# Optimization experiments

Hardware: AMD Instinct MI355X
Metric: run time of the kernel (lower is better)

Reference implementation:

```python
import jax, jax.numpy as jnp
import numpy as np
from jax import lax

# Conv4d decomposed (as in the torch implementation) into a sum of Conv3d's
# over the first spatial kernel axis. Each 3D conv is vectorized by folding
# the strided first-dim slices into the batch dimension.

def conv4d(x, w, b, stride=(2, 2, 2, 2), padding=(1, 1, 1, 1)):
    # x: [B, Ci, D1, D2, D3, D4]; w: [Co, Ci, K1, K2, K3, K4]; b: [Co]
    B, Ci, D1, D2, D3, D4 = x.shape
    Co, _, K1, K2, K3, K4 = w.shape
    s1, p1 = stride[0], padding[0]
    T = (D1 + 2 * p1 - K1) // s1 + 1  # output size along first spatial dim
    xp = jnp.pad(x, ((0, 0), (0, 0), (p1, p1), (0, 0), (0, 0), (0, 0)))
    pad3 = [(padding[j], padding[j]) for j in (1, 2, 3)]
    out = None
    for i in range(K1):  # small fixed loop over kernel taps along dim0
        xi = xp[:, :, i:i + s1 * (T - 1) + 1:s1]           # [B, Ci, T, D2, D3, D4]
        xi = jnp.moveaxis(xi, 2, 1).reshape(B * T, Ci, D2, D3, D4)
        yi = lax.conv_general_dilated(
            xi, w[:, :, i], window_strides=stride[1:], padding=pad3,
            dimension_numbers=('NCDHW', 'OIDHW', 'NCDHW'))
        out = yi if out is None else out + yi
    O2, O3, O4 = out.shape[2], out.shape[3], out.shape[4]
    out = out.reshape(B, T, Co, O2, O3, O4)
    out = jnp.moveaxis(out, 1, 2)                          # [B, Co, T, O2, O3, O4]
    return out + b[None, :, None, None, None, None]


def setup_inputs() -> dict:
    key = jax.random.key(0)
    k0, k1, k2, k3, k4 = jax.random.split(key, 5)
    C, R = 16, 4  # in_channel, mlp_ratio
    H = C * R     # 64
    x = jax.random.normal(k0, (1, C, 32, 32, 32, 32), dtype=jnp.float32)
    w1 = jax.random.normal(k1, (H, C, 3, 3, 3, 3), dtype=jnp.float32) * 0.02
    b1 = jax.random.normal(k2, (H,), dtype=jnp.float32) * 0.02
    w2 = jax.random.normal(k3, (C, H, 3, 3, 3, 3), dtype=jnp.float32) * 0.02
    b2 = jax.random.normal(k4, (C,), dtype=jnp.float32) * 0.02
    return {'x': x, 'w1': w1, 'b1': b1, 'w2': w2, 'b2': b2}


def reference(x, w1, b1, w2, b2):
    h = conv4d(x, w1, b1)                      # [1, 64, 16, 16, 16, 16]
    h = jax.nn.gelu(h, approximate=False)      # exact erf GELU (torch default)
    return conv4d(h, w2, b2)                   # [1, 16, 8, 8, 8, 8]
```

## Files before the change

### kernel.cpp

```cpp
#include <hip/hip_runtime.h>
#include <hip/hip_bf16.h>
#include <math.h>


typedef __attribute__((ext_vector_type(8))) short short8;
typedef __attribute__((ext_vector_type(4))) float f32x4;
typedef __attribute__((ext_vector_type(4))) unsigned int uint4v;

__device__ __forceinline__ unsigned short f2bf(float v) {
    __hip_bfloat16 b = __float2bfloat16(v);
    return *(unsigned short*)&b;
}

__global__ void setup_kernel(const float* __restrict__ w1, const float* __restrict__ w2,
                             const float* __restrict__ b2,
                             unsigned short* __restrict__ w1p, unsigned short* __restrict__ w2p,
                             uint4v* __restrict__ hz, float* __restrict__ out) {
    int b = blockIdx.x, tid = threadIdx.x;
    if (b < 544) {
        int i = b * 256 + tid;
        int kp = i % 136, co = (i / 136) & 63, ci = i / 8704;
        float v = 0.f;
        if (kp < 108 && (kp & 3) < 3) v = w1[(co * 16 + ci) * 81 + (kp >> 2) * 3 + (kp & 3)];
        w1p[i] = f2bf(v);
    } else if (b < 1088) {
        int i = (b - 544) * 256 + tid;
        int kp = i % 136, co = (i / 136) & 15, ci = i / 2176;
        float v = 0.f;
        if (kp < 108 && (kp & 3) < 3) v = w2[(co * 64 + ci) * 81 + (kp >> 2) * 3 + (kp & 3)];
        w2p[i] = f2bf(v);
    } else if (b < 1344) {
        int i = (b - 1088) * 256 + tid;
        out[i] = b2[i >> 12];
    } else {
        int i = (b - 1344) * 256 + tid;
        hz[i] = (uint4v){0, 0, 0, 0};
        int j = i + 704512;
        if (j < 839808) hz[j] = (uint4v){0, 0, 0, 0};
    }
}

__global__ __launch_bounds__(256) void conv1_mfma(
        const float* __restrict__ x, const unsigned short* __restrict__ w1p,
        const float* __restrict__ b1, unsigned short* __restrict__ hpad) {
    __shared__ unsigned short sX[36000];

    const int tid = threadIdx.x;
    const int bid = blockIdx.x;
    const int t4 = bid & 1, t3 = (bid >> 1) & 7, t2 = (bid >> 4) & 7, t1 = bid >> 7;
    const int bo1 = 2 * t1, bo2 = 2 * t2, bo3 = 2 * t3, bo4 = 8 * t4;
    const int g1b = 2 * bo1 - 1, g2b = 2 * bo2 - 1, g3b = 2 * bo3 - 1, g4b = 2 * bo4 - 1;

    int offs[5], swb[5];
    unsigned mka = 0, mkb = 0;
#pragma unroll
    for (int r = 0; r < 5; ++r) {
        int u = tid + 256 * r;
        bool uok = u < 1125;
        int uu = uok ? u : 0;
        int p = uu % 9, q = uu / 9;
        int i3 = q % 5; q /= 5;
        int i2 = q % 5; int i1 = q / 5;
        int g1 = g1b + i1, g2 = g2b + i2, g3 = g3b + i3;
        bool ok123 = uok & ((unsigned)g1 < 32u) & ((unsigned)g2 < 32u) & ((unsigned)g3 < 32u);
        int g4a = g4b + 2 * p;
        offs[r] = ((g1 * 32 + g2) * 32 + g3) * 32 + g4a;
        if (ok123 && (unsigned)g4a < 32u) mka |= 1u << r;
        if (ok123 && (unsigned)(g4a + 1) < 32u) mkb |= 1u << r;
        swb[r] = 2 * (((i1 * 5 + i2) * 5 + i3) * 18 + 2 * p);
    }

    {
        float fa[5], fb[5], na[5], nb[5];
#pragma unroll
        for (int r = 0; r < 5; ++r) {
            float va = 0.f, vb = 0.f;
            if ((mka >> r) & 1) va = x[offs[r]];
            if ((mkb >> r) & 1) vb = x[offs[r] + 1];
            fa[r] = va; fb[r] = vb;
        }
        for (int ci = 0; ci < 16; ++ci) {
            if (ci < 15) {
                const float* xc = x + (size_t)(ci + 1) * 1048576;
#pragma unroll
                for (int r = 0; r < 5; ++r) {
                    float va = 0.f, vb = 0.f;
                    if ((mka >> r) & 1) va = xc[offs[r]];
                    if ((mkb >> r) & 1) vb = xc[offs[r] + 1];
                    na[r] = va; nb[r] = vb;
                }
            }
            char* slab = (char*)sX + ci * 4500;
#pragma unroll
            for (int r = 0; r < 4; ++r)
                *(unsigned*)(slab + swb[r]) =
                    (unsigned)f2bf(fa[r]) | ((unsigned)f2bf(fb[r]) << 16);
            if (tid < 101)
                *(unsigned*)(slab + swb[4]) =
                    (unsigned)f2bf(fa[4]) | ((unsigned)f2bf(fb[4]) << 16);
            if (ci < 15) {
#pragma unroll
                for (int r = 0; r < 5; ++r) { fa[r] = na[r]; fb[r] = nb[r]; }
            }
        }
    }
    __syncthreads();

    const int lane = tid & 63, wv = tid >> 6;
    const int n16 = lane & 15, hi = lane >> 4;
    const int ct0 = 2 * (wv & 1);
    const int st0 = 2 * (wv >> 1);

    int fpb[2];
#pragma unroll
    for (int tt = 0; tt < 2; ++tt) {
        int sp = (st0 + tt) * 16 + n16;
        int o4l = sp & 7, o3l = (sp >> 3) & 1, o2l = (sp >> 4) & 1, o1l = sp >> 5;
        fpb[tt] = 2 * (900 * o1l + 180 * o2l + 36 * o3l + 2 * o4l);
    }
    int kof[4][2];
#pragma unroll
    for (int ks = 0; ks < 4; ++ks)
#pragma unroll
    for (int j = 0; j < 2; ++j) {
        int g = 8 * ks + 2 * hi + j;
        if (g > 26) g = 26;
        int k1 = g / 9, k2 = (g / 3) % 3, k3 = g % 3;
        kof[ks][j] = 2 * (450 * k1 + 90 * k2 + 18 * k3);
    }

    auto loadA = [&](int ci, short8 (&Ac)[8]) {
        const unsigned short* aw0 = w1p + (size_t)(ci * 64 + 16 * ct0 + n16) * 136 + hi * 8;
#pragma unroll
        for (int k = 0; k < 4; ++k) Ac[k] = *(const short8*)(aw0 + 32 * k);
        const unsigned short* aw1 = aw0 + 16 * 136;
#pragma unroll
        for (int k = 0; k < 4; ++k) Ac[4 + k] = *(const short8*)(aw1 + 32 * k);
    };

    f32x4 acc[2][2];
#pragma unroll
    for (int c = 0; c < 2; ++c)
#pragma unroll
    for (int t = 0; t < 2; ++t) acc[c][t] = (f32x4){0.f, 0.f, 0.f, 0.f};

    short8 A0[8], A1[8];
    loadA(0, A0);
    loadA(1, A1);

    auto kbody = [&](int ci, short8 (&Ac)[8]) {
        const char* sx = (const char*)sX + ci * 4500;
        short8 fr[2][4];
#pragma unroll
        for (int tt = 0; tt < 2; ++tt) {
            const char* base = sx + fpb[tt];
#pragma unroll
            for (int ks = 0; ks < 4; ++ks) {
                unsigned r0 = *(const unsigned*)(base + kof[ks][0]);
                unsigned r1 = *(const unsigned*)(base + kof[ks][0] + 4);
                unsigned r2 = *(const unsigned*)(base + kof[ks][1]);
                unsigned r3 = *(const unsigned*)(base + kof[ks][1] + 4);
                uint4v tmp = (uint4v){r0, r1, r2, r3};
                fr[tt][ks] = *(short8*)&tmp;
            }
        }
#pragma unroll
        for (int tt = 0; tt < 2; ++tt)
#pragma unroll
        for (int ks = 0; ks < 4; ++ks) {
            acc[0][tt] = __builtin_amdgcn_mfma_f32_16x16x32_bf16(Ac[ks],     fr[tt][ks], acc[0][tt], 0, 0, 0);
            acc[1][tt] = __builtin_amdgcn_mfma_f32_16x16x32_bf16(Ac[4 + ks], fr[tt][ks], acc[1][tt], 0, 0, 0);
        }
        if (ci < 14) loadA(ci + 2, Ac);
    };

    for (int cc = 0; cc < 16; cc += 2) {
        kbody(cc, A0);
        kbody(cc + 1, A1);
    }

#pragma unroll
    for (int c = 0; c < 2; ++c) {
#pragma unroll
        for (int tt = 0; tt < 2; ++tt) {
            int spl = 16 * (st0 + tt) + n16;
            int e4 = spl & 7, e3 = (spl >> 3) & 1, e2 = (spl >> 4) & 1, e1 = spl >> 5;
            size_t base = (size_t)(bo1 + e1 + 1) * 5832 + (bo2 + e2 + 1) * 324 +
                          (bo3 + e3 + 1) * 18 + (bo4 + e4 + 1);
#pragma unroll
            for (int r = 0; r < 4; ++r) {
                int co = 16 * (ct0 + c) + 4 * hi + r;
                float v = acc[c][tt][r] + b1[co];
                v = 0.5f * v * (1.f + erff(v * 0.70710678118654752f));
                hpad[(size_t)co * 104976 + base] = f2bf(v);
            }
        }
    }
}

__global__ __launch_bounds__(256) void conv2_mfma(
        const unsigned short* __restrict__ hpad, const unsigned short* __restrict__ w2p,
        float* __restrict__ out) {
    __shared__ unsigned short sX[18000];

    const int tid = threadIdx.x;
    const int bid = blockIdx.x;
    const int s = bid & 63, cig = bid >> 6;
    const int t3 = s & 3, t2 = (s >> 2) & 3, t1 = s >> 4;
    const int bo1 = 2 * t1, bo2 = 2 * t2, bo3 = 2 * t3;

    int offs[5], swb[5];
#pragma unroll
    for (int r = 0; r < 5; ++r) {
        int u = tid + 256 * r;
        if (u >= 1125) u = 0;
        int p = u % 9, q = u / 9;
        int i3 = q % 5; q /= 5;
        int i2 = q % 5; int i1 = q / 5;
        offs[r] = (2 * bo1 + i1) * 5832 + (2 * bo2 + i2) * 324 + (2 * bo3 + i3) * 18 + 2 * p;
        swb[r] = 2 * (((i1 * 5 + i2) * 5 + i3) * 18 + 2 * p);
    }

    {
        unsigned fa[5], na[5];
        const unsigned short* h0 = hpad + (size_t)(cig * 8) * 104976;
#pragma unroll
        for (int r = 0; r < 5; ++r) fa[r] = *(const unsigned*)(h0 + offs[r]);
        for (int s8 = 0; s8 < 8; ++s8) {
            if (s8 < 7) {
                const unsigned short* hc = hpad + (size_t)(cig * 8 + s8 + 1) * 104976;
#pragma unroll
                for (int r = 0; r < 5; ++r) na[r] = *(const unsigned*)(hc + offs[r]);
            }
            char* slab = (char*)sX + s8 * 4500;
#pragma unroll
            for (int r = 0; r < 4; ++r) *(unsigned*)(slab + swb[r]) = fa[r];
            if (tid < 101) *(unsigned*)(slab + swb[4]) = fa[4];
            if (s8 < 7) {
#pragma unroll
                for (int r = 0; r < 5; ++r) fa[r] = na[r];
            }
        }
    }
    __syncthreads();

    const int lane = tid & 63, wv = tid >> 6;
    const int n16 = lane & 15, hi = lane >> 4;

    int fpb;
    {
        int sp = wv * 16 + n16;
        int o4l = sp & 7, o3l = (sp >> 3) & 1, o2l = (sp >> 4) & 1, o1l = sp >> 5;
        fpb = 2 * (900 * o1l + 180 * o2l + 36 * o3l + 2 * o4l);
    }
    int kof[4][2];
#pragma unroll
    for (int ks = 0; ks < 4; ++ks)
#pragma unroll
    for (int j = 0; j < 2; ++j) {
        int g = 8 * ks + 2 * hi + j;
        if (g > 26) g = 26;
        int k1 = g / 9, k2 = (g / 3) % 3, k3 = g % 3;
        kof[ks][j] = 2 * (450 * k1 + 90 * k2 + 18 * k3);
    }

    auto loadA = [&](int s8, short8 (&Ac)[4]) {
        const unsigned short* aw = w2p + (size_t)((cig * 8 + s8) * 16 + n16) * 136 + hi * 8;
#pragma unroll
        for (int k = 0; k < 4; ++k) Ac[k] = *(const short8*)(aw + 32 * k);
    };

    f32x4 acc = (f32x4){0.f, 0.f, 0.f, 0.f};
    short8 A0[4], A1[4];
    loadA(0, A0);
    loadA(1, A1);

    auto kbody = [&](int s8, short8 (&Ac)[4]) {
        const char* base = (const char*)sX + s8 * 4500 + fpb;
        short8 fr[4];
#pragma unroll
        for (int ks = 0; ks < 4; ++ks) {
            unsigned r0 = *(const unsigned*)(base + kof[ks][0]);
            unsigned r1 = *(const unsigned*)(base + kof[ks][0] + 4);
            unsigned r2 = *(const unsigned*)(base + kof[ks][1]);
            unsigned r3 = *(const unsigned*)(base + kof[ks][1] + 4);
            uint4v tmp = (uint4v){r0, r1, r2, r3};
            fr[ks] = *(short8*)&tmp;
        }
#pragma unroll
        for (int ks = 0; ks < 4; ++ks)
            acc = __builtin_amdgcn_mfma_f32_16x16x32_bf16(Ac[ks], fr[ks], acc, 0, 0, 0);
        if (s8 < 6) loadA(s8 + 2, Ac);
    };

    for (int cc = 0; cc < 8; cc += 2) {
        kbody(cc, A0);
        kbody(cc + 1, A1);
    }

    {
        int spl = 16 * wv + n16;
        int e4 = spl & 7, e3 = (spl >> 3) & 1, e2 = (spl >> 4) & 1, e1 = spl >> 5;
        int o1 = bo1 + e1, o2 = bo2 + e2, o3 = bo3 + e3, o4 = e4;
#pragma unroll
        for (int r = 0; r < 4; ++r) {
            int co = 4 * hi + r;
            atomicAdd(&out[(size_t)co * 4096 + o1 * 512 + o2 * 64 + o3 * 8 + o4], acc[r]);
        }
    }
}

extern "C" void kernel_launch(void* const* d_in, const int* in_sizes, int n_in,
                              void* d_out, int out_size, void* d_ws, size_t ws_size,
                              hipStream_t stream) {
    const float* x  = (const float*)d_in[0];
    const float* w1 = (const float*)d_in[1];
    const float* b1 = (const float*)d_in[2];
    const float* w2 = (const float*)d_in[3];
    const float* b2 = (const float*)d_in[4];
    float* out = (float*)d_out;

    unsigned short* hpad = (unsigned short*)d_ws;
    unsigned short* w1p  = hpad + 6718464;
    unsigned short* w2p  = w1p + 139264;

    setup_kernel<<<4096, 256, 0, stream>>>(w1, w2, b2, w1p, w2p, (uint4v*)hpad, out);
    conv1_mfma<<<1024, 256, 0, stream>>>(x, w1p, b1, hpad);
    conv2_mfma<<<512, 256, 0, stream>>>(hpad, w2p, out);
}
```

Before: 86.63 us.

## Halve conv1 output tile per block to double grid and raise occupancy

Conv1 now gives each block a 2x2x2x4 output tile instead of 2x2x2x8, which shrinks the shared-memory input slab and doubles the grid to 2048 blocks. Each wave now owns one spatial tile and two channel tiles, so per-wave accumulators and fragment registers drop. Launch bounds request 4 blocks per CU, and the shared-memory B-fragment reads are software-pipelined across channels. The aim is more resident waves to hide gather and LDS latency, at the cost of more redundant halo loads from global memory and more weight-fragment reloads per output.

```diff
diff --git a/kernel.cpp b/kernel.cpp
--- a/kernel.cpp
+++ b/kernel.cpp
@@ -40,85 +40,75 @@
     }
 }
 
-__global__ __launch_bounds__(256) void conv1_mfma(
+__global__ __launch_bounds__(256, 4) void conv1_mfma(
         const float* __restrict__ x, const unsigned short* __restrict__ w1p,
         const float* __restrict__ b1, unsigned short* __restrict__ hpad) {
-    __shared__ unsigned short sX[36000];
+    __shared__ unsigned short sX[16 * 1256];
 
     const int tid = threadIdx.x;
     const int bid = blockIdx.x;
-    const int t4 = bid & 1, t3 = (bid >> 1) & 7, t2 = (bid >> 4) & 7, t1 = bid >> 7;
-    const int bo1 = 2 * t1, bo2 = 2 * t2, bo3 = 2 * t3, bo4 = 8 * t4;
+    const int t4 = bid & 3, t3 = (bid >> 2) & 7, t2 = (bid >> 5) & 7, t1 = bid >> 8;
+    const int bo1 = 2 * t1, bo2 = 2 * t2, bo3 = 2 * t3, bo4 = 4 * t4;
     const int g1b = 2 * bo1 - 1, g2b = 2 * bo2 - 1, g3b = 2 * bo3 - 1, g4b = 2 * bo4 - 1;
 
-    int offs[5], swb[5];
+    int offs[3], swb[3];
     unsigned mka = 0, mkb = 0;
 #pragma unroll
-    for (int r = 0; r < 5; ++r) {
+    for (int r = 0; r < 3; ++r) {
         int u = tid + 256 * r;
-        bool uok = u < 1125;
+        bool uok = u < 625;
         int uu = uok ? u : 0;
-        int p = uu % 9, q = uu / 9;
+        int p = uu % 5, q = uu / 5;
         int i3 = q % 5; q /= 5;
         int i2 = q % 5; int i1 = q / 5;
         int g1 = g1b + i1, g2 = g2b + i2, g3 = g3b + i3;
         bool ok123 = uok & ((unsigned)g1 < 32u) & ((unsigned)g2 < 32u) & ((unsigned)g3 < 32u);
         int g4a = g4b + 2 * p;
-        offs[r] = ((g1 * 32 + g2) * 32 + g3) * 32 + g4a;
+        offs[r] = ok123 ? ((g1 * 32 + g2) * 32 + g3) * 32 + g4a : 0;
         if (ok123 && (unsigned)g4a < 32u) mka |= 1u << r;
         if (ok123 && (unsigned)(g4a + 1) < 32u) mkb |= 1u << r;
-        swb[r] = 2 * (((i1 * 5 + i2) * 5 + i3) * 18 + 2 * p);
-    }
+        swb[r] = 2 * (((i1 * 5 + i2) * 5 + i3) * 10 + 2 * p);
+    }
+
+    auto gatherX = [&](int ci, float (&a)[3], float (&b)[3]) {
+        const float* xc = x + (size_t)ci * 1048576;
+#pragma unroll
+        for (int r = 0; r < 3; ++r) {
+            float va = 0.f, vb = 0.f;
+            if ((mka >> r) & 1) va = xc[offs[r]];
+            if ((mkb >> r) & 1) vb = xc[offs[r] + 1];
+            a[r] = va; b[r] = vb;
+        }
+    };
+    auto writeSlab = [&](int ci, const float (&a)[3], const float (&b)[3]) {
+        char* slab = (char*)sX + ci * 2512;
+#pragma unroll
+        for (int r = 0; r < 2; ++r)
+            *(unsigned*)(slab + swb[r]) = (unsigned)f2bf(a[r]) | ((unsigned)f2bf(b[r]) << 16);
+        if (tid < 113)
+            *(unsigned*)(slab + swb[2]) = (unsigned)f2bf(a[2]) | ((unsigned)f2bf(b[2]) << 16);
+    };
 
     {
-        float fa[5], fb[5], na[5], nb[5];
-#pragma unroll
-        for (int r = 0; r < 5; ++r) {
-            float va = 0.f, vb = 0.f;
-            if ((mka >> r) & 1) va = x[offs[r]];
-            if ((mkb >> r) & 1) vb = x[offs[r] + 1];
-            fa[r] = va; fb[r] = vb;
-        }
-        for (int ci = 0; ci < 16; ++ci) {
-            if (ci < 15) {
-                const float* xc = x + (size_t)(ci + 1) * 1048576;
-#pragma unroll
-                for (int r = 0; r < 5; ++r) {
-                    float va = 0.f, vb = 0.f;
-                    if ((mka >> r) & 1) va = xc[offs[r]];
-                    if ((mkb >> r) & 1) vb = xc[offs[r] + 1];
-                    na[r] = va; nb[r] = vb;
-                }
-            }
-            char* slab = (char*)sX + ci * 4500;
-#pragma unroll
-            for (int r = 0; r < 4; ++r)
-                *(unsigned*)(slab + swb[r]) =
-                    (unsigned)f2bf(fa[r]) | ((unsigned)f2bf(fb[r]) << 16);
-            if (tid < 101)
-                *(unsigned*)(slab + swb[4]) =
-                    (unsigned)f2bf(fa[4]) | ((unsigned)f2bf(fb[4]) << 16);
-            if (ci < 15) {
-#pragma unroll
-                for (int r = 0; r < 5; ++r) { fa[r] = na[r]; fb[r] = nb[r]; }
-            }
+        float a0[3], b0[3], a1[3], b1v[3];
+        gatherX(0, a0, b0);
+        gatherX(1, a1, b1v);
+        for (int cc = 0; cc < 16; cc += 2) {
+            writeSlab(cc, a0, b0);
+            if (cc + 2 < 16) gatherX(cc + 2, a0, b0);
+            writeSlab(cc + 1, a1, b1v);
+            if (cc + 3 < 16) gatherX(cc + 3, a1, b1v);
         }
     }
     __syncthreads();
 
     const int lane = tid & 63, wv = tid >> 6;
     const int n16 = lane & 15, hi = lane >> 4;
-    const int ct0 = 2 * (wv & 1);
-    const int st0 = 2 * (wv >> 1);
-
-    int fpb[2];
-#pragma unroll
-    for (int tt = 0; tt < 2; ++tt) {
-        int sp = (st0 + tt) * 16 + n16;
-        int o4l = sp & 7, o3l = (sp >> 3) & 1, o2l = (sp >> 4) & 1, o1l = sp >> 5;
-        fpb[tt] = 2 * (900 * o1l + 180 * o2l + 36 * o3l + 2 * o4l);
-    }
-    int kof[4][2];
+    const int stile = wv & 1;
+    const int ct0 = 2 * (wv >> 1);
+
+    const int fpb = 1000 * stile + 200 * ((n16 >> 3) & 1) + 40 * ((n16 >> 2) & 1) + 4 * (n16 & 3);
+    int kofB[4][2];
 #pragma unroll
     for (int ks = 0; ks < 4; ++ks)
 #pragma unroll
@@ -126,7 +116,7 @@
         int g = 8 * ks + 2 * hi + j;
         if (g > 26) g = 26;
         int k1 = g / 9, k2 = (g / 3) % 3, k3 = g % 3;
-        kof[ks][j] = 2 * (450 * k1 + 90 * k2 + 18 * k3);
+        kofB[ks][j] = 500 * k1 + 100 * k2 + 20 * k3;
     }
 
     auto loadA = [&](int ci, short8 (&Ac)[8]) {
@@ -137,63 +127,55 @@
 #pragma unroll
         for (int k = 0; k < 4; ++k) Ac[4 + k] = *(const short8*)(aw1 + 32 * k);
     };
-
-    f32x4 acc[2][2];
-#pragma unroll
-    for (int c = 0; c < 2; ++c)
-#pragma unroll
-    for (int t = 0; t < 2; ++t) acc[c][t] = (f32x4){0.f, 0.f, 0.f, 0.f};
-
-    short8 A0[8], A1[8];
+    auto readFR = [&](int ci, short8 (&fr)[4]) {
+        const char* base = (const char*)sX + ci * 2512 + fpb;
+#pragma unroll
+        for (int ks = 0; ks < 4; ++ks) {
+            unsigned r0 = *(const unsigned*)(base + kofB[ks][0]);
+            unsigned r1 = *(const unsigned*)(base + kofB[ks][0] + 4);
+            unsigned r2 = *(const unsigned*)(base + kofB[ks][1]);
+            unsigned r3 = *(const unsigned*)(base + kofB[ks][1] + 4);
+            uint4v t = (uint4v){r0, r1, r2, r3};
+            fr[ks] = *(short8*)&t;
+        }
+    };
+
+    f32x4 acc[2];
+    acc[0] = (f32x4){0.f, 0.f, 0.f, 0.f};
+    acc[1] = (f32x4){0.f, 0.f, 0.f, 0.f};
+
+    auto mfma8 = [&](const short8 (&Ac)[8], const short8 (&fr)[4]) {
+#pragma unroll
+        for (int ks = 0; ks < 4; ++ks) {
+            acc[0] = __builtin_amdgcn_mfma_f32_16x16x32_bf16(Ac[ks],     fr[ks], acc[0], 0, 0, 0);
+            acc[1] = __builtin_amdgcn_mfma_f32_16x16x32_bf16(Ac[4 + ks], fr[ks], acc[1], 0, 0, 0);
+        }
+    };
+
+    short8 A0[8], A1[8], F0[4], F1[4];
     loadA(0, A0);
     loadA(1, A1);
-
-    auto kbody = [&](int ci, short8 (&Ac)[8]) {
-        const char* sx = (const char*)sX + ci * 4500;
-        short8 fr[2][4];
-#pragma unroll
-        for (int tt = 0; tt < 2; ++tt) {
-            const char* base = sx + fpb[tt];
-#pragma unroll
-            for (int ks = 0; ks < 4; ++ks) {
-                unsigned r0 = *(const unsigned*)(base + kof[ks][0]);
-                unsigned r1 = *(const unsigned*)(base + kof[ks][0] + 4);
-                unsigned r2 = *(const unsigned*)(base + kof[ks][1]);
-                unsigned r3 = *(const unsigned*)(base + kof[ks][1] + 4);
-                uint4v tmp = (uint4v){r0, r1, r2, r3};
-                fr[tt][ks] = *(short8*)&tmp;
-            }
-        }
-#pragma unroll
-        for (int tt = 0; tt < 2; ++tt)
-#pragma unroll
-        for (int ks = 0; ks < 4; ++ks) {
-            acc[0][tt] = __builtin_amdgcn_mfma_f32_16x16x32_bf16(Ac[ks],     fr[tt][ks], acc[0][tt], 0, 0, 0);
-            acc[1][tt] = __builtin_amdgcn_mfma_f32_16x16x32_bf16(Ac[4 + ks], fr[tt][ks], acc[1][tt], 0, 0, 0);
-        }
-        if (ci < 14) loadA(ci + 2, Ac);
-    };
+    readFR(0, F0);
 
     for (int cc = 0; cc < 16; cc += 2) {
-        kbody(cc, A0);
-        kbody(cc + 1, A1);
-    }
-
+        if (cc < 15) readFR(cc + 1, F1);
+        mfma8(A0, F0);
+        if (cc < 14) { loadA(cc + 2, A0); readFR(cc + 2, F0); }
+        mfma8(A1, F1);
+        if (cc < 14) loadA(cc + 3, A1);
+    }
+
+    const int e4 = n16 & 3, e3 = (n16 >> 2) & 1, e2 = (n16 >> 3) & 1, e1 = stile;
+    const size_t base = (size_t)(bo1 + e1 + 1) * 5832 + (bo2 + e2 + 1) * 324 +
+                        (bo3 + e3 + 1) * 18 + (bo4 + e4 + 1);
 #pragma unroll
     for (int c = 0; c < 2; ++c) {
 #pragma unroll
-        for (int tt = 0; tt < 2; ++tt) {
-            int spl = 16 * (st0 + tt) + n16;
-            int e4 = spl & 7, e3 = (spl >> 3) & 1, e2 = (spl >> 4) & 1, e1 = spl >> 5;
-            size_t base = (size_t)(bo1 + e1 + 1) * 5832 + (bo2 + e2 + 1) * 324 +
-                          (bo3 + e3 + 1) * 18 + (bo4 + e4 + 1);
-#pragma unroll
-            for (int r = 0; r < 4; ++r) {
-                int co = 16 * (ct0 + c) + 4 * hi + r;
-                float v = acc[c][tt][r] + b1[co];
-                v = 0.5f * v * (1.f + erff(v * 0.70710678118654752f));
-                hpad[(size_t)co * 104976 + base] = f2bf(v);
-            }
+        for (int r = 0; r < 4; ++r) {
+            int co = 16 * (ct0 + c) + 4 * hi + r;
+            float v = acc[c][r] + b1[co];
+            v = 0.5f * v * (1.f + erff(v * 0.70710678118654752f));
+            hpad[(size_t)co * 104976 + base] = f2bf(v);
         }
     }
 }
@@ -325,6 +307,6 @@
     unsigned short* w2p  = w1p + 139264;
 
     setup_kernel<<<4096, 256, 0, stream>>>(w1, w2, b2, w1p, w2p, (uint4v*)hpad, out);
-    conv1_mfma<<<1024, 256, 0, stream>>>(x, w1p, b1, hpad);
+    conv1_mfma<<<2048, 256, 0, stream>>>(x, w1p, b1, hpad);
     conv2_mfma<<<512, 256, 0, stream>>>(hpad, w2p, out);
 }
```

New measurement: 148.7 us, median of 2. 1.72x slower.
